# Performance work log

Measured on AMD Instinct MI355X. Metric: run time of the kernel, lower is better.

The kernel has to match this reference:

```python
import jax, jax.numpy as jnp
import numpy as np

B, S, H = 1, 1024, 1024
E = 1024          # expert_dim
NEXP = 16         # num_experts
TOPK = 2
ALPHA = 1.702
LIMIT = 7.0


def setup_inputs() -> dict:
    key = jax.random.key(0)
    ks = jax.random.split(key, 8)
    hidden_states = jax.random.normal(ks[0], (B, S, H), dtype=jnp.float32)
    # router (gate): Linear(H, NEXP) with bias
    Wg = jax.random.normal(ks[1], (NEXP, H), dtype=jnp.float32) / np.sqrt(H)
    bg = jax.random.normal(ks[2], (NEXP,), dtype=jnp.float32) * 0.01
    # per-expert gate_up_proj: Linear(H, 2E) -> store as [NEXP, H, 2E]
    Wgu = jax.random.normal(ks[3], (NEXP, H, 2 * E), dtype=jnp.float32) / np.sqrt(H)
    bgu = jax.random.normal(ks[4], (NEXP, 2 * E), dtype=jnp.float32) * 0.01
    # per-expert down_proj: Linear(E, H) -> store as [NEXP, E, H]
    Wd = jax.random.normal(ks[5], (NEXP, E, H), dtype=jnp.float32) / np.sqrt(E)
    bd = jax.random.normal(ks[6], (NEXP, H), dtype=jnp.float32) * 0.01
    return {"hidden_states": hidden_states, "Wg": Wg, "bg": bg,
            "Wgu": Wgu, "bgu": bgu, "Wd": Wd, "bd": bd}


def _moe_forward(x, Wg, bg, Wgu, bgu, Wd, bd):
    b, s, h = x.shape
    xt = x.reshape(-1, h)                                   # [T, H]
    # router
    logits = xt @ Wg.T + bg                                 # [T, NEXP]
    # gpt_oss routing: topk over raw logits, softmax over selected
    top_vals, top_idx = jax.lax.top_k(logits, TOPK)         # [T, K]
    rw = jax.nn.softmax(top_vals.astype(jnp.float32), axis=-1).astype(xt.dtype)
    # combine weight per (token, expert): zero for unselected experts
    onehot = jax.nn.one_hot(top_idx, NEXP, dtype=xt.dtype)  # [T, K, NEXP]
    cw = jnp.einsum("tk,tke->te", rw, onehot)               # [T, NEXP]
    # dense expert compute (reference math identical to gather/scatter version)
    gu = jnp.einsum("th,ehf->tef", xt, Wgu) + bgu[None]     # [T, NEXP, 2E]
    gate = gu[..., ::2]
    up = gu[..., 1::2]
    gate = jnp.minimum(gate, LIMIT)
    up = jnp.clip(up, -LIMIT, LIMIT)
    glu = gate * jax.nn.sigmoid(gate * ALPHA)
    gated = (up + 1.0) * glu                                # [T, NEXP, E]
    out_e = jnp.einsum("tef,efh->teh", gated, Wd) + bd[None]  # [T, NEXP, H]
    out = jnp.einsum("teh,te->th", out_e, cw)               # [T, H]
    return out.reshape(b, s, h)


def reference(hidden_states, Wg, bg, Wgu, bgu, Wd, bd):
    return _moe_forward(hidden_states, Wg, bg, Wgu, bgu, Wd, bd)
```

## Files before the change

### kernel.cpp

```cpp
#include <hip/hip_runtime.h>
#include <hip/hip_bf16.h>

#define NT 1024
#define HD 1024
#define ED 1024
#define F2D 2048
#define NEXPERT 16
#define GROWS 2304
#define ALPHA_C 1.702f
#define LIMIT_C 7.0f

typedef float f32x4 __attribute__((ext_vector_type(4)));
typedef float fv4 __attribute__((ext_vector_type(4)));
typedef short short8 __attribute__((ext_vector_type(8)));
typedef unsigned int u32x4 __attribute__((ext_vector_type(4)));

__device__ __forceinline__ unsigned short f2bf(float x) {
  union { float f; unsigned int u; } v; v.f = x;
  unsigned int r = v.u + 0x7FFFu + ((v.u >> 16) & 1u);
  return (unsigned short)(r >> 16);
}
__device__ __forceinline__ unsigned int pk2(float lo, float hi) {
  return (unsigned int)f2bf(lo) | ((unsigned int)f2bf(hi) << 16);
}
__device__ __forceinline__ fv4 ldnt4(const float* p) {
  return __builtin_nontemporal_load((const fv4*)p);
}
__device__ __forceinline__ void async16(const void* g, void* l) {
  __builtin_amdgcn_global_load_lds((const __attribute__((address_space(1))) void*)g,
                                   (__attribute__((address_space(3))) void*)l, 16, 0, 0);
}

__global__ __launch_bounds__(256) void k_router(const float* __restrict__ x,
                                                const float* __restrict__ Wg,
                                                const float* __restrict__ bg,
                                                const float* __restrict__ bd,
                                                int* __restrict__ e01,
                                                float* __restrict__ w0f,
                                                float* __restrict__ w1f,
                                                unsigned short* __restrict__ Xbf,
                                                float* __restrict__ out) {
  const int t = blockIdx.x;
  const int tid = threadIdx.x;
  const int w = tid >> 6;
  const int l = tid & 63;
  const float4* x4 = (const float4*)(x + (size_t)t * HD);
  {
    float4 v = x4[tid];
    unsigned int* dst = (unsigned int*)(Xbf + (size_t)t * HD + tid * 4);
    dst[0] = pk2(v.x, v.y); dst[1] = pk2(v.z, v.w);
  }
  const int e = l & 15, qq = l >> 4;
  const float4* wg4 = (const float4*)(Wg + (size_t)e * HD);
  float s = 0.f;
#pragma unroll 4
  for (int j = 0; j < 16; ++j) {
    const int idx = w * 64 + qq + 4 * j;
    float4 a = x4[idx], b = wg4[idx];
    s += a.x * b.x + a.y * b.y + a.z * b.z + a.w * b.w;
  }
  s += __shfl_xor(s, 16);
  s += __shfl_xor(s, 32);
  __shared__ float slog[4][16];
  if (l < 16) slog[w][e] = s;
  __syncthreads();
  float v0 = -1e30f, v1 = -1e30f; int i0 = 0, i1 = 0;
  for (int k2 = 0; k2 < 16; ++k2) {
    float lv = slog[0][k2] + slog[1][k2] + slog[2][k2] + slog[3][k2] + bg[k2];
    if (lv > v0) { v1 = v0; i1 = i0; v0 = lv; i0 = k2; }
    else if (lv > v1) { v1 = lv; i1 = k2; }
  }
  const float w0 = 1.f / (1.f + __expf(v1 - v0));
  const float w1 = 1.f - w0;
  if (tid == 0) {
    e01[t] = i0 | (i1 << 8);
    w0f[t] = w0;
    w1f[t] = w1;
  }
  const float4* bd0 = (const float4*)(bd + (size_t)i0 * HD);
  const float4* bd1 = (const float4*)(bd + (size_t)i1 * HD);
  float4 a = bd0[tid], b = bd1[tid];
  float4 r;
  r.x = w0 * a.x + w1 * b.x;
  r.y = w0 * a.y + w1 * b.y;
  r.z = w0 * a.z + w1 * b.z;
  r.w = w0 * a.w + w1 * b.w;
  ((float4*)(out + (size_t)t * HD))[tid] = r;
}

__global__ __launch_bounds__(1024) void k_scan(const int* __restrict__ e01,
                                               const float* __restrict__ w0f,
                                               const float* __restrict__ w1f,
                                               int* __restrict__ cnt,
                                               int* __restrict__ off,
                                               int* __restrict__ gtok,
                                               float* __restrict__ gwt) {
  __shared__ int scnt[NEXPERT];
  __shared__ int soff[NEXPERT];
  __shared__ int scur[NEXPERT];
  const int t = threadIdx.x;
  if (t < NEXPERT) { scnt[t] = 0; scur[t] = 0; }
  __syncthreads();
  const int p = e01[t];
  const int e0 = p & 255, e1 = p >> 8;
  atomicAdd(&scnt[e0], 1);
  atomicAdd(&scnt[e1], 1);
  __syncthreads();
  if (t == 0) {
    int a = 0;
    for (int e = 0; e < NEXPERT; ++e) { soff[e] = a; off[e] = a; cnt[e] = scnt[e]; a += scnt[e]; }
  }
  __syncthreads();
  int s0 = atomicAdd(&scur[e0], 1);
  gtok[soff[e0] + s0] = t; gwt[soff[e0] + s0] = w0f[t];
  int s1 = atomicAdd(&scur[e1], 1);
  gtok[soff[e1] + s1] = t; gwt[soff[e1] + s1] = w1f[t];
}

#define BSTG1 132
__global__ __launch_bounds__(512, 1) void k_gemm1(const unsigned short* __restrict__ Xbf,
                                                  const float* __restrict__ Wgu,
                                                  const float* __restrict__ bgu,
                                                  const int* __restrict__ cnt,
                                                  const int* __restrict__ off,
                                                  const int* __restrict__ gtok,
                                                  unsigned short* __restrict__ Gact) {
  const int e = blockIdx.z;
  const int Ne = cnt[e];
  const int mtile = blockIdx.y;
  if (mtile * 256 >= Ne) return;
  const int ntile = blockIdx.x;
  const int tid = threadIdx.x;
  const int lane = tid & 63;
  const int wv = tid >> 6;
  const int wm = wv >> 1;
  const int wn = wv & 1;
  const int q = lane >> 4;
  const int fr = lane & 15;
  const int base = off[e] + mtile * 256;

  __shared__ unsigned short Alds[2][256 * 32];
  __shared__ unsigned int Blds[2][16 * BSTG1];

  const int ar0 = wv * 32 + (lane >> 2);
  const int ar1 = ar0 + 16;
  const int ags0 = base + (((mtile * 256 + ar0) < Ne) ? ar0 : 0);
  const int ags1 = base + (((mtile * 256 + ar1) < Ne) ? ar1 : 0);
  const unsigned short* agp0 = Xbf + (size_t)gtok[ags0] * HD + (lane & 3) * 8;
  const unsigned short* agp1 = Xbf + (size_t)gtok[ags1] * HD + (lane & 3) * 8;
  const int aofs = wv * 1024;

  const int p2 = tid >> 5;
  const int bc = tid & 31;
  const float* Wb = Wgu + (size_t)e * HD * F2D + (size_t)(2 * p2) * F2D + ntile * 128 + bc * 4;

  f32x4 acc[4][4] = {};
  fv4 b0, b1;

  b0 = ldnt4(Wb);
  b1 = ldnt4(Wb + F2D);
  async16(agp0, Alds[0] + aofs);
  async16(agp1, Alds[0] + aofs + 512);
  {
    u32x4 pkv;
    pkv[0] = pk2(b0[0], b1[0]); pkv[1] = pk2(b0[1], b1[1]);
    pkv[2] = pk2(b0[2], b1[2]); pkv[3] = pk2(b0[3], b1[3]);
    *(u32x4*)(Blds[0] + p2 * BSTG1 + bc * 4) = pkv;
  }
  __syncthreads();

  for (int ks = 0; ks < 32; ++ks) {
    const int cur = ks & 1, nxt = cur ^ 1;
    const bool more = (ks + 1) < 32;
    if (more) {
      const float* bp = Wb + (size_t)(ks + 1) * 32 * F2D;
      b0 = ldnt4(bp);
      b1 = ldnt4(bp + F2D);
      async16(agp0 + (ks + 1) * 32, Alds[nxt] + aofs);
      async16(agp1 + (ks + 1) * 32, Alds[nxt] + aofs + 512);
    }
    short8 af[4], bfr[4];
#pragma unroll
    for (int mi = 0; mi < 4; ++mi)
      af[mi] = *(const short8*)(Alds[cur] + (wm * 64 + mi * 16 + fr) * 32 + q * 8);
#pragma unroll
    for (int ni = 0; ni < 4; ++ni) {
      const unsigned int* p = Blds[cur] + (q * 4) * BSTG1 + wn * 64 + ni * 16 + fr;
      union { unsigned int u[4]; short8 s; } uu;
      uu.u[0] = p[0]; uu.u[1] = p[BSTG1]; uu.u[2] = p[2 * BSTG1]; uu.u[3] = p[3 * BSTG1];
      bfr[ni] = uu.s;
    }
#pragma unroll
    for (int mi = 0; mi < 4; ++mi)
#pragma unroll
      for (int ni = 0; ni < 4; ++ni)
        acc[mi][ni] = __builtin_amdgcn_mfma_f32_16x16x32_bf16(af[mi], bfr[ni], acc[mi][ni], 0, 0, 0);
    if (more) {
      u32x4 pkv;
      pkv[0] = pk2(b0[0], b1[0]); pkv[1] = pk2(b0[1], b1[1]);
      pkv[2] = pk2(b0[2], b1[2]); pkv[3] = pk2(b0[3], b1[3]);
      *(u32x4*)(Blds[nxt] + p2 * BSTG1 + bc * 4) = pkv;
    }
    __syncthreads();
  }

  const float* bguE = bgu + (size_t)e * F2D + ntile * 128;
#pragma unroll
  for (int mi = 0; mi < 4; ++mi) {
#pragma unroll
    for (int ni = 0; ni < 4; ++ni) {
      const int coll = wn * 64 + ni * 16 + fr;
      const float bias = bguE[coll];
#pragma unroll
      for (int r = 0; r < 4; ++r) {
        const int srow = wm * 64 + mi * 16 + q * 4 + r;
        float v = acc[mi][ni][r] + bias;
        float pv = __shfl_xor(v, 1);
        float gate = (lane & 1) ? pv : v;
        float up   = (lane & 1) ? v : pv;
        gate = fminf(gate, LIMIT_C);
        up = fminf(fmaxf(up, -LIMIT_C), LIMIT_C);
        float glu = gate / (1.f + __expf(-ALPHA_C * gate));
        float val = (up + 1.f) * glu;
        if (!(lane & 1) && (mtile * 256 + srow) < Ne)
          Gact[(size_t)(base + srow) * ED + ((ntile * 128 + coll) >> 1)] = f2bf(val);
      }
    }
  }
}

#define BSTG2T 20
__global__ __launch_bounds__(512, 2) void k_gemm2(const unsigned short* __restrict__ Gact,
                                                  const float* __restrict__ Wd,
                                                  const int* __restrict__ cnt,
                                                  const int* __restrict__ off,
                                                  const int* __restrict__ gtok,
                                                  const float* __restrict__ gwt,
                                                  float* __restrict__ out) {
  const int e = blockIdx.z;
  const int Ne = cnt[e];
  const int mtile = blockIdx.y;
  if (mtile * 256 >= Ne) return;
  const int ntile = blockIdx.x;
  const int tid = threadIdx.x;
  const int lane = tid & 63;
  const int wv = tid >> 6;
  const int q = lane >> 4;
  const int fr = lane & 15;
  const int base = off[e] + mtile * 256;

  __shared__ unsigned short Alds[2][256 * 32];
  __shared__ unsigned int Blds[2][64 * BSTG2T];

  const int ar0 = wv * 32 + (lane >> 2);
  const unsigned short* agp0 = Gact + (size_t)(base + ar0) * ED + (lane & 3) * 8;
  const unsigned short* agp1 = agp0 + (size_t)16 * ED;
  const int aofs = wv * 1024;

  const int sub = lane & 3;
  const float* Wb = Wd + (size_t)e * ED * HD + (size_t)(2 * (wv * 4 + sub)) * HD + ntile * 64 + (lane >> 2) * 4;

  f32x4 acc[2][4] = {};
  fv4 b0, b1;

#define B2_TRANSPOSE_STORE(BUF)                                                         \
  {                                                                                     \
    unsigned int w0p = pk2(b0[0], b1[0]);                                               \
    unsigned int w1p = pk2(b0[1], b1[1]);                                               \
    unsigned int w2p = pk2(b0[2], b1[2]);                                               \
    unsigned int w3p = pk2(b0[3], b1[3]);                                               \
    unsigned int X0 = sub == 0 ? w0p : sub == 1 ? w1p : sub == 2 ? w2p : w3p;           \
    unsigned int X1 = sub == 0 ? w1p : sub == 1 ? w0p : sub == 2 ? w3p : w2p;           \
    unsigned int X2 = sub == 0 ? w2p : sub == 1 ? w3p : sub == 2 ? w0p : w1p;           \
    unsigned int X3 = sub == 0 ? w3p : sub == 1 ? w2p : sub == 2 ? w1p : w0p;           \
    unsigned int r0 = X0;                                                               \
    unsigned int r1 = (unsigned int)__builtin_amdgcn_update_dpp((int)X1, (int)X1, 0xB1, 0xF, 0xF, 0); \
    unsigned int r2 = (unsigned int)__builtin_amdgcn_update_dpp((int)X2, (int)X2, 0x4E, 0xF, 0xF, 0); \
    unsigned int r3 = (unsigned int)__builtin_amdgcn_update_dpp((int)X3, (int)X3, 0x1B, 0xF, 0xF, 0); \
    u32x4 tt;                                                                           \
    tt[0] = sub == 0 ? r0 : sub == 1 ? r1 : sub == 2 ? r2 : r3;                         \
    tt[1] = sub == 0 ? r1 : sub == 1 ? r0 : sub == 2 ? r3 : r2;                         \
    tt[2] = sub == 0 ? r2 : sub == 1 ? r3 : sub == 2 ? r0 : r1;                         \
    tt[3] = sub == 0 ? r3 : sub == 1 ? r2 : sub == 2 ? r1 : r0;                         \
    *(u32x4*)(Blds[BUF] + lane * BSTG2T + wv * 4) = tt;                                 \
  }

  if (tid < 256) {
    b0 = ldnt4(Wb);
    b1 = ldnt4(Wb + HD);
  }
  async16(agp0, Alds[0] + aofs);
  async16(agp1, Alds[0] + aofs + 512);
  if (tid < 256) B2_TRANSPOSE_STORE(0)
  __syncthreads();

  for (int ks = 0; ks < 32; ++ks) {
    const int cur = ks & 1, nxt = cur ^ 1;
    const bool more = (ks + 1) < 32;
    if (more) {
      if (tid < 256) {
        const float* bp = Wb + (size_t)(ks + 1) * 32 * HD;
        b0 = ldnt4(bp);
        b1 = ldnt4(bp + HD);
      }
      async16(agp0 + (ks + 1) * 32, Alds[nxt] + aofs);
      async16(agp1 + (ks + 1) * 32, Alds[nxt] + aofs + 512);
    }
    short8 af[2], bfr[4];
#pragma unroll
    for (int mi = 0; mi < 2; ++mi)
      af[mi] = *(const short8*)(Alds[cur] + (wv * 32 + mi * 16 + fr) * 32 + q * 8);
#pragma unroll
    for (int ni = 0; ni < 4; ++ni)
      bfr[ni] = *(const short8*)(Blds[cur] + (ni * 16 + fr) * BSTG2T + q * 4);
#pragma unroll
    for (int mi = 0; mi < 2; ++mi)
#pragma unroll
      for (int ni = 0; ni < 4; ++ni)
        acc[mi][ni] = __builtin_amdgcn_mfma_f32_16x16x32_bf16(af[mi], bfr[ni], acc[mi][ni], 0, 0, 0);
    if (more && tid < 256) B2_TRANSPOSE_STORE(nxt)
    __syncthreads();
  }

#pragma unroll
  for (int mi = 0; mi < 2; ++mi) {
#pragma unroll
    for (int r = 0; r < 4; ++r) {
      const int srow = wv * 32 + mi * 16 + q * 4 + r;
      if ((mtile * 256 + srow) < Ne) {
        const int gsl = base + srow;
        const int tok = gtok[gsl];
        const float wt = gwt[gsl];
        float* op = out + (size_t)tok * HD + ntile * 64;
#pragma unroll
        for (int ni = 0; ni < 4; ++ni) {
          const int col = ni * 16 + fr;
          atomicAdd(op + col, wt * acc[mi][ni][r]);
        }
      }
    }
  }
}

extern "C" void kernel_launch(void* const* d_in, const int* in_sizes, int n_in,
                              void* d_out, int out_size, void* d_ws, size_t ws_size,
                              hipStream_t stream) {
  const float* x   = (const float*)d_in[0];
  const float* Wg  = (const float*)d_in[1];
  const float* bg  = (const float*)d_in[2];
  const float* Wgu = (const float*)d_in[3];
  const float* bgu = (const float*)d_in[4];
  const float* Wd  = (const float*)d_in[5];
  const float* bd  = (const float*)d_in[6];
  float* out = (float*)d_out;

  int* cnt = (int*)d_ws;
  int* off = cnt + 16;
  int* e01 = off + 16;
  float* w0f = (float*)(e01 + NT);
  float* w1f = w0f + NT;
  int* gtok = (int*)(w1f + NT);
  float* gwt = (float*)(gtok + GROWS);
  unsigned short* Xbf = (unsigned short*)(gwt + GROWS);
  unsigned short* Gact = Xbf + (size_t)NT * HD;

  k_router<<<NT, 256, 0, stream>>>(x, Wg, bg, bd, e01, w0f, w1f, Xbf, out);
  k_scan<<<1, NT, 0, stream>>>(e01, w0f, w1f, cnt, off, gtok, gwt);
  k_gemm1<<<dim3(16, 2, NEXPERT), 512, 0, stream>>>(Xbf, Wgu, bgu, cnt, off, gtok, Gact);
  k_gemm2<<<dim3(16, 2, NEXPERT), 512, 0, stream>>>(Gact, Wd, cnt, off, gtok, gwt, out);
}
```

Baseline: 330.8 us.

## Transpose B tile in LDS for gemm1 and load gemm2 A fragments directly to registers

In gemm1, the weight tile is now stored in LDS in a column-major (transposed) layout using DPP lane swaps. MFMA B fragments can then be read with a single 128-bit LDS load instead of four strided 32-bit loads. In gemm2, the A operand (activations) no longer goes through LDS; each lane loads its fragment straight from global memory into registers, prefetched one step ahead. This removes LDS traffic and scattered reads, at the cost of extra DPP/select work and uncoalesced 16-byte global loads for A in gemm2.

```diff
diff --git a/kernel.cpp b/kernel.cpp
--- a/kernel.cpp
+++ b/kernel.cpp
@@ -30,6 +30,28 @@
   __builtin_amdgcn_global_load_lds((const __attribute__((address_space(1))) void*)g,
                                    (__attribute__((address_space(3))) void*)l, 16, 0, 0);
 }
+
+#define BT_TRANSPOSE_STORE(DST)                                                         \
+  {                                                                                     \
+    unsigned int w0p = pk2(b0[0], b1[0]);                                               \
+    unsigned int w1p = pk2(b0[1], b1[1]);                                               \
+    unsigned int w2p = pk2(b0[2], b1[2]);                                               \
+    unsigned int w3p = pk2(b0[3], b1[3]);                                               \
+    unsigned int X0 = sub == 0 ? w0p : sub == 1 ? w1p : sub == 2 ? w2p : w3p;           \
+    unsigned int X1 = sub == 0 ? w1p : sub == 1 ? w0p : sub == 2 ? w3p : w2p;           \
+    unsigned int X2 = sub == 0 ? w2p : sub == 1 ? w3p : sub == 2 ? w0p : w1p;           \
+    unsigned int X3 = sub == 0 ? w3p : sub == 1 ? w2p : sub == 2 ? w1p : w0p;           \
+    unsigned int r0 = X0;                                                               \
+    unsigned int r1 = (unsigned int)__builtin_amdgcn_update_dpp((int)X1, (int)X1, 0xB1, 0xF, 0xF, 0); \
+    unsigned int r2 = (unsigned int)__builtin_amdgcn_update_dpp((int)X2, (int)X2, 0x4E, 0xF, 0xF, 0); \
+    unsigned int r3 = (unsigned int)__builtin_amdgcn_update_dpp((int)X3, (int)X3, 0x1B, 0xF, 0xF, 0); \
+    u32x4 tt;                                                                           \
+    tt[0] = sub == 0 ? r0 : sub == 1 ? r1 : sub == 2 ? r2 : r3;                         \
+    tt[1] = sub == 0 ? r1 : sub == 1 ? r0 : sub == 2 ? r3 : r2;                         \
+    tt[2] = sub == 0 ? r2 : sub == 1 ? r3 : sub == 2 ? r0 : r1;                         \
+    tt[3] = sub == 0 ? r3 : sub == 1 ? r2 : sub == 2 ? r1 : r0;                         \
+    *(u32x4*)(DST) = tt;                                                                \
+  }
 
 __global__ __launch_bounds__(256) void k_router(const float* __restrict__ x,
                                                 const float* __restrict__ Wg,
@@ -117,7 +139,7 @@
   gtok[soff[e1] + s1] = t; gwt[soff[e1] + s1] = w1f[t];
 }
 
-#define BSTG1 132
+#define BSTG1T 20
 __global__ __launch_bounds__(512, 1) void k_gemm1(const unsigned short* __restrict__ Xbf,
                                                   const float* __restrict__ Wgu,
                                                   const float* __restrict__ bgu,
@@ -140,7 +162,7 @@
   const int base = off[e] + mtile * 256;
 
   __shared__ unsigned short Alds[2][256 * 32];
-  __shared__ unsigned int Blds[2][16 * BSTG1];
+  __shared__ unsigned int Blds[2][128 * BSTG1T];
 
   const int ar0 = wv * 32 + (lane >> 2);
   const int ar1 = ar0 + 16;
@@ -150,9 +172,12 @@
   const unsigned short* agp1 = Xbf + (size_t)gtok[ags1] * HD + (lane & 3) * 8;
   const int aofs = wv * 1024;
 
-  const int p2 = tid >> 5;
-  const int bc = tid & 31;
-  const float* Wb = Wgu + (size_t)e * HD * F2D + (size_t)(2 * p2) * F2D + ntile * 128 + bc * 4;
+  const int sub = tid & 3;
+  const int qd = tid >> 2;
+  const int kblock = qd >> 5;
+  const int colgrp = qd & 31;
+  const float* Wb = Wgu + (size_t)e * HD * F2D + (size_t)(2 * (kblock * 4 + sub)) * F2D + ntile * 128 + colgrp * 4;
+  const int bofs = (colgrp * 4 + sub) * BSTG1T + kblock * 4;
 
   f32x4 acc[4][4] = {};
   fv4 b0, b1;
@@ -161,12 +186,7 @@
   b1 = ldnt4(Wb + F2D);
   async16(agp0, Alds[0] + aofs);
   async16(agp1, Alds[0] + aofs + 512);
-  {
-    u32x4 pkv;
-    pkv[0] = pk2(b0[0], b1[0]); pkv[1] = pk2(b0[1], b1[1]);
-    pkv[2] = pk2(b0[2], b1[2]); pkv[3] = pk2(b0[3], b1[3]);
-    *(u32x4*)(Blds[0] + p2 * BSTG1 + bc * 4) = pkv;
-  }
+  BT_TRANSPOSE_STORE(Blds[0] + bofs)
   __syncthreads();
 
   for (int ks = 0; ks < 32; ++ks) {
@@ -184,23 +204,14 @@
     for (int mi = 0; mi < 4; ++mi)
       af[mi] = *(const short8*)(Alds[cur] + (wm * 64 + mi * 16 + fr) * 32 + q * 8);
 #pragma unroll
-    for (int ni = 0; ni < 4; ++ni) {
-      const unsigned int* p = Blds[cur] + (q * 4) * BSTG1 + wn * 64 + ni * 16 + fr;
-      union { unsigned int u[4]; short8 s; } uu;
-      uu.u[0] = p[0]; uu.u[1] = p[BSTG1]; uu.u[2] = p[2 * BSTG1]; uu.u[3] = p[3 * BSTG1];
-      bfr[ni] = uu.s;
-    }
+    for (int ni = 0; ni < 4; ++ni)
+      bfr[ni] = *(const short8*)(Blds[cur] + (wn * 64 + ni * 16 + fr) * BSTG1T + q * 4);
 #pragma unroll
     for (int mi = 0; mi < 4; ++mi)
 #pragma unroll
       for (int ni = 0; ni < 4; ++ni)
         acc[mi][ni] = __builtin_amdgcn_mfma_f32_16x16x32_bf16(af[mi], bfr[ni], acc[mi][ni], 0, 0, 0);
-    if (more) {
-      u32x4 pkv;
-      pkv[0] = pk2(b0[0], b1[0]); pkv[1] = pk2(b0[1], b1[1]);
-      pkv[2] = pk2(b0[2], b1[2]); pkv[3] = pk2(b0[3], b1[3]);
-      *(u32x4*)(Blds[nxt] + p2 * BSTG1 + bc * 4) = pkv;
-    }
+    if (more) BT_TRANSPOSE_STORE(Blds[nxt] + bofs)
     __syncthreads();
   }
 
@@ -249,49 +260,26 @@
   const int fr = lane & 15;
   const int base = off[e] + mtile * 256;
 
-  __shared__ unsigned short Alds[2][256 * 32];
   __shared__ unsigned int Blds[2][64 * BSTG2T];
 
-  const int ar0 = wv * 32 + (lane >> 2);
-  const unsigned short* agp0 = Gact + (size_t)(base + ar0) * ED + (lane & 3) * 8;
-  const unsigned short* agp1 = agp0 + (size_t)16 * ED;
-  const int aofs = wv * 1024;
+  const unsigned short* agA0 = Gact + (size_t)(base + wv * 32 + fr) * ED + q * 8;
+  const unsigned short* agA1 = agA0 + (size_t)16 * ED;
 
   const int sub = lane & 3;
   const float* Wb = Wd + (size_t)e * ED * HD + (size_t)(2 * (wv * 4 + sub)) * HD + ntile * 64 + (lane >> 2) * 4;
+  const int bofs = lane * BSTG2T + wv * 4;
 
   f32x4 acc[2][4] = {};
   fv4 b0, b1;
-
-#define B2_TRANSPOSE_STORE(BUF)                                                         \
-  {                                                                                     \
-    unsigned int w0p = pk2(b0[0], b1[0]);                                               \
-    unsigned int w1p = pk2(b0[1], b1[1]);                                               \
-    unsigned int w2p = pk2(b0[2], b1[2]);                                               \
-    unsigned int w3p = pk2(b0[3], b1[3]);                                               \
-    unsigned int X0 = sub == 0 ? w0p : sub == 1 ? w1p : sub == 2 ? w2p : w3p;           \
-    unsigned int X1 = sub == 0 ? w1p : sub == 1 ? w0p : sub == 2 ? w3p : w2p;           \
-    unsigned int X2 = sub == 0 ? w2p : sub == 1 ? w3p : sub == 2 ? w0p : w1p;           \
-    unsigned int X3 = sub == 0 ? w3p : sub == 1 ? w2p : sub == 2 ? w1p : w0p;           \
-    unsigned int r0 = X0;                                                               \
-    unsigned int r1 = (unsigned int)__builtin_amdgcn_update_dpp((int)X1, (int)X1, 0xB1, 0xF, 0xF, 0); \
-    unsigned int r2 = (unsigned int)__builtin_amdgcn_update_dpp((int)X2, (int)X2, 0x4E, 0xF, 0xF, 0); \
-    unsigned int r3 = (unsigned int)__builtin_amdgcn_update_dpp((int)X3, (int)X3, 0x1B, 0xF, 0xF, 0); \
-    u32x4 tt;                                                                           \
-    tt[0] = sub == 0 ? r0 : sub == 1 ? r1 : sub == 2 ? r2 : r3;                         \
-    tt[1] = sub == 0 ? r1 : sub == 1 ? r0 : sub == 2 ? r3 : r2;                         \
-    tt[2] = sub == 0 ? r2 : sub == 1 ? r3 : sub == 2 ? r0 : r1;                         \
-    tt[3] = sub == 0 ? r3 : sub == 1 ? r2 : sub == 2 ? r1 : r0;                         \
-    *(u32x4*)(Blds[BUF] + lane * BSTG2T + wv * 4) = tt;                                 \
-  }
+  short8 a0, a1, a0n, a1n;
 
   if (tid < 256) {
     b0 = ldnt4(Wb);
     b1 = ldnt4(Wb + HD);
   }
-  async16(agp0, Alds[0] + aofs);
-  async16(agp1, Alds[0] + aofs + 512);
-  if (tid < 256) B2_TRANSPOSE_STORE(0)
+  a0 = *(const short8*)(agA0);
+  a1 = *(const short8*)(agA1);
+  if (tid < 256) BT_TRANSPOSE_STORE(Blds[0] + bofs)
   __syncthreads();
 
   for (int ks = 0; ks < 32; ++ks) {
@@ -303,23 +291,22 @@
         b0 = ldnt4(bp);
         b1 = ldnt4(bp + HD);
       }
-      async16(agp0 + (ks + 1) * 32, Alds[nxt] + aofs);
-      async16(agp1 + (ks + 1) * 32, Alds[nxt] + aofs + 512);
-    }
-    short8 af[2], bfr[4];
-#pragma unroll
-    for (int mi = 0; mi < 2; ++mi)
-      af[mi] = *(const short8*)(Alds[cur] + (wv * 32 + mi * 16 + fr) * 32 + q * 8);
+      a0n = *(const short8*)(agA0 + (ks + 1) * 32);
+      a1n = *(const short8*)(agA1 + (ks + 1) * 32);
+    }
+    short8 bfr[4];
 #pragma unroll
     for (int ni = 0; ni < 4; ++ni)
       bfr[ni] = *(const short8*)(Blds[cur] + (ni * 16 + fr) * BSTG2T + q * 4);
 #pragma unroll
-    for (int mi = 0; mi < 2; ++mi)
-#pragma unroll
-      for (int ni = 0; ni < 4; ++ni)
-        acc[mi][ni] = __builtin_amdgcn_mfma_f32_16x16x32_bf16(af[mi], bfr[ni], acc[mi][ni], 0, 0, 0);
-    if (more && tid < 256) B2_TRANSPOSE_STORE(nxt)
+    for (int ni = 0; ni < 4; ++ni) {
+      acc[0][ni] = __builtin_amdgcn_mfma_f32_16x16x32_bf16(a0, bfr[ni], acc[0][ni], 0, 0, 0);
+      acc[1][ni] = __builtin_amdgcn_mfma_f32_16x16x32_bf16(a1, bfr[ni], acc[1][ni], 0, 0, 0);
+    }
+    if (more && tid < 256) BT_TRANSPOSE_STORE(Blds[nxt] + bofs)
     __syncthreads();
+    a0 = a0n;
+    a1 = a1n;
   }
 
 #pragma unroll
```

New measurement: 339.7 us. 2.7% more time.
